# Kernel optimization log

Measured on AMD Instinct MI355X. Metric: run time of the kernel, lower is better.

The kernel has to match this reference:

```python
import jax, jax.numpy as jnp
import numpy as np

FREQUENCY_COUNT = 16

def setup_inputs() -> dict:
    key = jax.random.key(0)
    k1, k2 = jax.random.split(key)
    x = jax.random.normal(k1, (4096, 1024), dtype=jnp.float32)
    coef = jax.random.normal(k2, (1024, 1024, 2 * FREQUENCY_COUNT + 1), dtype=jnp.float32) * 0.1
    return {"x": x, "coef": coef}

def _fourier_features(x, K):
    ks = jnp.arange(1, K + 1, dtype=x.dtype)            # [K]
    ang = x[:, :, None] * ks[None, None, :]             # [B, I, K]
    ones = jnp.ones(x.shape + (1,), dtype=x.dtype)      # [B, I, 1]
    return jnp.concatenate([jnp.sin(ang), jnp.cos(ang), ones], axis=2)

def reference(x, coef):
    K = (coef.shape[-1] - 1) // 2
    values = _fourier_features(x, K)                     # [B, I, 2K+1]
    # sum over input dim i and frequency dim k, weighted per output j
    return jnp.einsum("oik,bik->bo", coef, values)      # [B, O]
```

## Files before the change

kernel.cpp:

```cpp
#include <hip/hip_runtime.h>


#define O_COLS 1024
#define I_DIM  1024
#define NF33   33
#define B_ROWS 4096

#define CW2_BYTES  ((size_t)32 * 2048 * 512 * 2)
#define XT_OFF     (CW2_BYTES)
#define XT_BYTES   ((size_t)I_DIM * B_ROWS * 4)
#define BK_OFF     (XT_OFF + XT_BYTES)
#define BK_BYTES   ((size_t)I_DIM * O_COLS * 4)
#define BIAS_OFF   (BK_OFF + BK_BYTES)
#define PART_OFF   (BIAS_OFF + (1 << 20))
#define PART_BYTES ((size_t)B_ROWS * O_COLS * 4)
#define NEED_T1    (PART_OFF + 3 * PART_BYTES)
#define NEED_T2    (BIAS_OFF + 4096)

#define ASTR 36

typedef _Float16 half8 __attribute__((ext_vector_type(8)));
typedef float f32x16 __attribute__((ext_vector_type(16)));
typedef float float4v __attribute__((ext_vector_type(4)));
union H8 { half8 v; _Float16 h[8]; };

#define BAR() asm volatile("s_waitcnt lgkmcnt(0)\n\ts_barrier" ::: "memory")

__device__ __forceinline__ int ksrc_of(int f) {
  return (f >= 32) ? 32 : ((f >> 1) + ((f & 1) ? 16 : 0));
}

__global__ __launch_bounds__(256)
void convert_coef2(const float* __restrict__ coef, _Float16* __restrict__ Cw2,
                   float* __restrict__ bk) {
  const int gtid = blockIdx.x * 256 + threadIdx.x;
  const int o = gtid & 1023;
  const int i = gtid >> 10;

  const float* src = coef + (size_t)o * (I_DIM * NF33) + (size_t)i * NF33;
  float r[NF33];
#pragma unroll
  for (int k = 0; k < NF33; ++k) r[k] = src[k];

  const int ob32 = o >> 5;
#pragma unroll
  for (int kcl = 0; kcl < 2; ++kcl) {
#pragma unroll
    for (int kh = 0; kh < 2; ++kh) {
      H8 h;
#pragma unroll
      for (int e = 0; e < 8; ++e)
        h.h[e] = (_Float16)r[ksrc_of(kcl * 16 + kh * 8 + e)];
      const size_t blob = (size_t)ob32 * 2048 + (size_t)i * 2 + kcl;
      *(half8*)(Cw2 + blob * 512 + (kh * 32 + (o & 31)) * 8) = h.v;
    }
  }
  bk[(size_t)i * 1024 + o] = r[32];
}

__global__ __launch_bounds__(256)
void transpose_x(const float* __restrict__ x, float* __restrict__ xT) {
  __shared__ float t[64][65];
  const int bi = blockIdx.x;
  const int bj = blockIdx.y;
  const int tx = threadIdx.x & 63, ty = threadIdx.x >> 6;
#pragma unroll
  for (int mq = 0; mq < 16; ++mq) {
    const int r = mq * 4 + ty;
    t[r][tx] = x[(size_t)(bj * 64 + r) * I_DIM + bi * 64 + tx];
  }
  __syncthreads();
#pragma unroll
  for (int mq = 0; mq < 16; ++mq) {
    const int r = mq * 4 + ty;
    xT[(size_t)(bi * 64 + r) * B_ROWS + bj * 64 + tx] = t[tx][r];
  }
}

__global__ __launch_bounds__(256)
void bias_from_bk(const float* __restrict__ bk, float* __restrict__ bias) {
  const int o = blockIdx.x * 256 + threadIdx.x;
  float s0 = 0.f, s1 = 0.f, s2 = 0.f, s3 = 0.f;
  for (int i = 0; i < 1024; i += 4) {
    s0 += bk[(size_t)i * 1024 + o];
    s1 += bk[(size_t)(i + 1) * 1024 + o];
    s2 += bk[(size_t)(i + 2) * 1024 + o];
    s3 += bk[(size_t)(i + 3) * 1024 + o];
  }
  bias[o] = (s0 + s1) + (s2 + s3);
}

__global__ __launch_bounds__(256)
void reduce_parts(float* __restrict__ out, const float* __restrict__ p0,
                  const float* __restrict__ p1, const float* __restrict__ p2) {
  const size_t i = ((size_t)blockIdx.x * 256 + threadIdx.x) * 4;
  float4v a = *(float4v*)(out + i);
  float4v b = *(const float4v*)(p0 + i);
  float4v c = *(const float4v*)(p1 + i);
  float4v d = *(const float4v*)(p2 + i);
  *(float4v*)(out + i) = a + b + c + d;
}

__device__ __forceinline__ void genH(float xv, _Float16* dst) {
  float S[17], C[17];
  __sincosf(xv, &S[1], &C[1]);
  S[2] = 2.f * S[1] * C[1];  C[2] = fmaf(-2.f * S[1], S[1], 1.f);
  S[3] = S[2] * C[1] + C[2] * S[1];  C[3] = C[2] * C[1] - S[2] * S[1];
  S[4] = 2.f * S[2] * C[2];  C[4] = fmaf(-2.f * S[2], S[2], 1.f);
  S[5] = S[4] * C[1] + C[4] * S[1];  C[5] = C[4] * C[1] - S[4] * S[1];
  S[6] = S[4] * C[2] + C[4] * S[2];  C[6] = C[4] * C[2] - S[4] * S[2];
  S[7] = S[4] * C[3] + C[4] * S[3];  C[7] = C[4] * C[3] - S[4] * S[3];
  S[8] = 2.f * S[4] * C[4];  C[8] = fmaf(-2.f * S[4], S[4], 1.f);
#pragma unroll
  for (int k = 1; k < 8; ++k) {
    S[8 + k] = S[8] * C[k] + C[8] * S[k];
    C[8 + k] = C[8] * C[k] - S[8] * S[k];
  }
  S[16] = 2.f * S[8] * C[8];  C[16] = fmaf(-2.f * S[8], S[8], 1.f);
#pragma unroll
  for (int c4 = 0; c4 < 4; ++c4) {
    H8 h;
#pragma unroll
    for (int q = 0; q < 4; ++q) {
      const int k = c4 * 4 + q + 1;
      h.h[2 * q] = (_Float16)S[k];  h.h[2 * q + 1] = (_Float16)C[k];
    }
    *(half8*)(dst + c4 * 8) = h.v;
  }
}

template <bool ATOMIC>
__global__ __launch_bounds__(384, 2)
void fourier_gemm10(const float* __restrict__ xT, const _Float16* __restrict__ Cw2,
                    const float* __restrict__ bias, float* __restrict__ out,
                    float* __restrict__ part) {
  __shared__ _Float16 As[2][4][128][ASTR];

  const int tid = threadIdx.x, lane = tid & 63, wave = tid >> 6;

  const int bid = blockIdx.x;
  const int g = bid & 15;
  const int m0 = (bid >> 4) * 128;
  const int n = g >> 2;
  const int kb = g & 3;
  const int o0 = n * 256;
  const int i0 = kb * 256;

  if (wave >= 4) {
    const int grow = tid - 256;
    const float* px = xT + (size_t)i0 * B_ROWS + (m0 + grow);

    {
      float x4[4];
#pragma unroll
      for (int c = 0; c < 4; ++c) x4[c] = px[(size_t)c * B_ROWS];
#pragma unroll
      for (int c = 0; c < 4; ++c) genH(x4[c], &As[0][c][grow][0]);
    }
    BAR();
#pragma unroll 1
    for (int p = 0; p < 64; ++p) {
      if (p < 63) {
        const int s1 = 4 * (p + 1);
        float x4[4];
#pragma unroll
        for (int c = 0; c < 4; ++c) x4[c] = px[(size_t)(s1 + c) * B_ROWS];
        _Float16* dstb = &As[(p & 1) ^ 1][0][grow][0];
#pragma unroll
        for (int c = 0; c < 4; ++c) genH(x4[c], dstb + c * (128 * ASTR));
      }
      BAR();
    }
    return;
  }

  const int wc = wave;
  const int r32 = lane & 31, kh = lane >> 5;

  const _Float16* pb0 = Cw2 + ((size_t)(n * 8 + wc * 2 + 0) * 2048 + (size_t)i0 * 2) * 512 + lane * 8;
  const _Float16* pb1 = Cw2 + ((size_t)(n * 8 + wc * 2 + 1) * 2048 + (size_t)i0 * 2) * 512 + lane * 8;

  f32x16 acc[4][2];
#pragma unroll
  for (int fr = 0; fr < 4; ++fr)
#pragma unroll
    for (int fc = 0; fc < 2; ++fc)
#pragma unroll
      for (int q = 0; q < 16; ++q) acc[fr][fc][q] = 0.f;
  if (kb == 0) {
#pragma unroll
    for (int fc = 0; fc < 2; ++fc) {
      const float bv = bias[o0 + wc * 64 + fc * 32 + r32];
#pragma unroll
      for (int fr = 0; fr < 4; ++fr)
#pragma unroll
        for (int q = 0; q < 16; ++q) acc[fr][fc][q] = bv;
    }
  }

  half8 B0[4], B1[4];
  auto loadB = [&](half8 (&Bt)[4], int s) {
    const size_t base = (size_t)(s * 2) * 512;
    Bt[0] = *(const half8*)(pb0 + base);
    Bt[1] = *(const half8*)(pb0 + base + 512);
    Bt[2] = *(const half8*)(pb1 + base);
    Bt[3] = *(const half8*)(pb1 + base + 512);
  };
  auto mfma_sub = [&](int buf, int col, const half8 (&Bt)[4]) {
    half8 a_[4][2];
#pragma unroll
    for (int fr = 0; fr < 4; ++fr)
#pragma unroll
      for (int kcl = 0; kcl < 2; ++kcl)
        a_[fr][kcl] = *(const half8*)&As[buf][col][fr * 32 + r32][(kcl * 2 + kh) * 8];
#pragma unroll
    for (int kcl = 0; kcl < 2; ++kcl)
#pragma unroll
      for (int fr = 0; fr < 4; ++fr)
#pragma unroll
        for (int fc = 0; fc < 2; ++fc)
          acc[fr][fc] = __builtin_amdgcn_mfma_f32_32x32x16_f16(
              a_[fr][kcl], Bt[fc * 2 + kcl], acc[fr][fc], 0, 0, 0);
  };

  loadB(B0, 0);
  BAR();

#pragma unroll 1
  for (int p = 0; p < 64; ++p) {
    const int buf = p & 1;
    const int s = 4 * p;
    loadB(B1, s + 1);
    mfma_sub(buf, 0, B0);
    loadB(B0, s + 2);
    mfma_sub(buf, 1, B1);
    loadB(B1, s + 3);
    mfma_sub(buf, 2, B0);
    if (p < 63) loadB(B0, s + 4);
    mfma_sub(buf, 3, B1);
    BAR();
  }

  float* dst;
  if (ATOMIC) dst = out;
  else dst = (kb == 0) ? out : part + (size_t)(kb - 1) * (B_ROWS * O_COLS);
#pragma unroll
  for (int fr = 0; fr < 4; ++fr)
#pragma unroll
    for (int fc = 0; fc < 2; ++fc)
#pragma unroll
      for (int q = 0; q < 16; ++q) {
        const int row = m0 + fr * 32 + (q & 3) + 8 * (q >> 2) + 4 * kh;
        const int col = o0 + wc * 64 + fc * 32 + r32;
        if (ATOMIC) atomicAdd(&dst[(size_t)row * O_COLS + col], acc[fr][fc][q]);
        else dst[(size_t)row * O_COLS + col] = acc[fr][fc][q];
      }
}

__global__ __launch_bounds__(512, 4)
void fourier_gemm_direct(const float* __restrict__ x, const float* __restrict__ coef,
                         float* __restrict__ out) {
  __shared__ _Float16 Asd[128 * 64];
  __shared__ _Float16 Bsd[128 * 64];

  const int tid = threadIdx.x;
  const int lane = tid & 63;
  const int wave = tid >> 6;
  const int wr = wave >> 1;
  const int wcd = wave & 1;

  const int bid = blockIdx.x;
  const int o0 = (bid & 7) * 128;
  const int kb = (bid >> 3) & 1;
  const int m0 = (bid >> 4) * 128;

  const int rowA = tid >> 3;
  const int cch = tid & 7;
  const int cswz = cch ^ (rowA & 7);
  const int n1 = tid >> 3;
  const int c1q = tid & 7;
  const int r16 = lane & 15;
  const int kq = lane >> 4;

  float4v acc[2][4];
#pragma unroll
  for (int fr = 0; fr < 2; ++fr)
#pragma unroll
    for (int fc = 0; fc < 4; ++fc) acc[fr][fc] = (float4v){0.f, 0.f, 0.f, 0.f};

  float s1a[8], c1a[8], sa[8], ca[8];
  float s1b[8], c1b[8], sb[8], cb[8];

  const float* xa_base = x + (size_t)(m0 + rowA) * I_DIM + (size_t)kb * 512 + cch * 8;
  const float* xb_base = xa_base + (size_t)64 * I_DIM;

#pragma unroll 1
  for (int ib2 = 0; ib2 < 8; ++ib2) {
    {
      const float* xa = xa_base + ib2 * 64;
      const float* xb = xb_base + ib2 * 64;
      float xva[8], xvb[8];
      *(float4*)&xva[0] = *(const float4*)(xa);
      *(float4*)&xva[4] = *(const float4*)(xa + 4);
      *(float4*)&xvb[0] = *(const float4*)(xb);
      *(float4*)&xvb[4] = *(const float4*)(xb + 4);
#pragma unroll
      for (int e = 0; e < 8; ++e) {
        __sincosf(xva[e], &s1a[e], &c1a[e]); sa[e] = s1a[e]; ca[e] = c1a[e];
        __sincosf(xvb[e], &s1b[e], &c1b[e]); sb[e] = s1b[e]; cb[e] = c1b[e];
      }
    }
#pragma unroll 1
    for (int f = 0; f < NF33; ++f) {
      H8 ha, hb;
      if (f == 32) {
#pragma unroll
        for (int e = 0; e < 8; ++e) { ha.h[e] = (_Float16)1.0f; hb.h[e] = (_Float16)1.0f; }
      } else if ((f & 1) == 0) {
#pragma unroll
        for (int e = 0; e < 8; ++e) { ha.h[e] = (_Float16)sa[e]; hb.h[e] = (_Float16)sb[e]; }
      } else {
#pragma unroll
        for (int e = 0; e < 8; ++e) { ha.h[e] = (_Float16)ca[e]; hb.h[e] = (_Float16)cb[e]; }
      }
      __syncthreads();
      {
        const int ks = ksrc_of(f);
        const int ibg = kb * 8 + ib2;
        H8 b1, b2;
#pragma unroll
        for (int e = 0; e < 8; ++e) {
          const size_t ii = (size_t)(ibg * 64 + c1q * 8 + e) * NF33 + ks;
          b1.h[e] = (_Float16)coef[(size_t)(o0 + n1) * (I_DIM * NF33) + ii];
          b2.h[e] = (_Float16)coef[(size_t)(o0 + n1 + 64) * (I_DIM * NF33) + ii];
        }
        const int cs = (c1q ^ (n1 & 7)) << 3;
        *(half8*)&Bsd[n1 * 64 + cs] = b1.v;
        *(half8*)&Bsd[(n1 + 64) * 64 + cs] = b2.v;
      }
      *(half8*)&Asd[rowA * 64 + cswz * 8] = ha.v;
      *(half8*)&Asd[(rowA + 64) * 64 + cswz * 8] = hb.v;
      if ((f & 1) && (f + 2 < NF33)) {
#pragma unroll
        for (int e = 0; e < 8; ++e) {
          float ns = sa[e] * c1a[e] + ca[e] * s1a[e];
          ca[e] = ca[e] * c1a[e] - sa[e] * s1a[e]; sa[e] = ns;
          float nsb = sb[e] * c1b[e] + cb[e] * s1b[e];
          cb[e] = cb[e] * c1b[e] - sb[e] * s1b[e]; sb[e] = nsb;
        }
      }
      __syncthreads();
#pragma unroll
      for (int ksu = 0; ksu < 2; ++ksu) {
        const int ch = ((ksu << 2) + kq) ^ (r16 & 7);
        half8 af[2], bf[4];
#pragma unroll
        for (int fr = 0; fr < 2; ++fr)
          af[fr] = *(const half8*)&Asd[(wr * 32 + fr * 16 + r16) * 64 + ch * 8];
#pragma unroll
        for (int fc = 0; fc < 4; ++fc)
          bf[fc] = *(const half8*)&Bsd[(wcd * 64 + fc * 16 + r16) * 64 + ch * 8];
#pragma unroll
        for (int fr = 0; fr < 2; ++fr)
#pragma unroll
          for (int fc = 0; fc < 4; ++fc)
            acc[fr][fc] = __builtin_amdgcn_mfma_f32_16x16x32_f16(
                af[fr], bf[fc], acc[fr][fc], 0, 0, 0);
      }
    }
  }
#pragma unroll
  for (int fr = 0; fr < 2; ++fr)
#pragma unroll
    for (int fc = 0; fc < 4; ++fc)
#pragma unroll
      for (int r = 0; r < 4; ++r) {
        const int row = m0 + wr * 32 + fr * 16 + kq * 4 + r;
        const int col = o0 + wcd * 64 + fc * 16 + r16;
        atomicAdd(&out[(size_t)row * O_COLS + col], acc[fr][fc][r]);
      }
}

extern "C" void kernel_launch(void* const* d_in, const int* in_sizes, int n_in,
                              void* d_out, int out_size, void* d_ws, size_t ws_size,
                              hipStream_t stream) {
  const float* x = (const float*)d_in[0];
  const float* coef = (const float*)d_in[1];
  float* out = (float*)d_out;

  if (ws_size >= NEED_T1 || ws_size >= NEED_T2) {
    _Float16* Cw2 = (_Float16*)d_ws;
    float* xT   = (float*)((char*)d_ws + XT_OFF);
    float* bk   = (float*)((char*)d_ws + BK_OFF);
    float* bias = (float*)((char*)d_ws + BIAS_OFF);
    convert_coef2<<<dim3(4096), dim3(256), 0, stream>>>(coef, Cw2, bk);
    transpose_x<<<dim3(16, 64), dim3(256), 0, stream>>>(x, xT);
    bias_from_bk<<<dim3(4), dim3(256), 0, stream>>>(bk, bias);
    if (ws_size >= NEED_T1) {
      float* part = (float*)((char*)d_ws + PART_OFF);
      fourier_gemm10<false><<<dim3(512), dim3(384), 0, stream>>>(xT, Cw2, bias, out, part);
      reduce_parts<<<dim3(4096), dim3(256), 0, stream>>>(
          out, part, part + (size_t)B_ROWS * O_COLS, part + (size_t)2 * B_ROWS * O_COLS);
    } else {
      hipMemsetAsync(out, 0, (size_t)B_ROWS * O_COLS * sizeof(float), stream);
      fourier_gemm10<true><<<dim3(512), dim3(384), 0, stream>>>(xT, Cw2, bias, out, nullptr);
    }
  } else {
    hipMemsetAsync(out, 0, (size_t)B_ROWS * O_COLS * sizeof(float), stream);
    fourier_gemm_direct<<<dim3(512), dim3(512), 0, stream>>>(x, coef, out);
  }
}
```

Before: 463.6 us.

## Merge feature-generation waves into MFMA waves and widen output tile

Removes the dedicated producer waves that computed Fourier features into shared memory. All eight waves now do MFMA work over a 512-column output tile, and each wave pair generates one feature column between its MFMA sub-steps, with x values prefetched one iteration ahead. The aim is to stop leaving two waves idle for matrix math and to reuse each A tile across twice as many output columns. The cost is higher register pressure at 512 threads per block and half as many blocks (256), which may leave CUs underfilled.

Result: faster. 422.3 us (-8.9%).

```diff
diff --git a/kernel.cpp b/kernel.cpp
--- a/kernel.cpp
+++ b/kernel.cpp
@@ -130,8 +130,8 @@
 }
 
 template <bool ATOMIC>
-__global__ __launch_bounds__(384, 2)
-void fourier_gemm10(const float* __restrict__ xT, const _Float16* __restrict__ Cw2,
+__global__ __launch_bounds__(512, 2)
+void fourier_gemm11(const float* __restrict__ xT, const _Float16* __restrict__ Cw2,
                     const float* __restrict__ bias, float* __restrict__ out,
                     float* __restrict__ part) {
   __shared__ _Float16 As[2][4][128][ASTR];
@@ -139,46 +139,22 @@
   const int tid = threadIdx.x, lane = tid & 63, wave = tid >> 6;
 
   const int bid = blockIdx.x;
-  const int g = bid & 15;
-  const int m0 = (bid >> 4) * 128;
-  const int n = g >> 2;
-  const int kb = g & 3;
-  const int o0 = n * 256;
+  const int g = bid & 7;
+  const int m0 = (bid >> 3) * 128;
+  const int n = g & 1;
+  const int kb = g >> 1;
+  const int o0 = n * 512;
   const int i0 = kb * 256;
 
-  if (wave >= 4) {
-    const int grow = tid - 256;
-    const float* px = xT + (size_t)i0 * B_ROWS + (m0 + grow);
-
-    {
-      float x4[4];
-#pragma unroll
-      for (int c = 0; c < 4; ++c) x4[c] = px[(size_t)c * B_ROWS];
-#pragma unroll
-      for (int c = 0; c < 4; ++c) genH(x4[c], &As[0][c][grow][0]);
-    }
-    BAR();
-#pragma unroll 1
-    for (int p = 0; p < 64; ++p) {
-      if (p < 63) {
-        const int s1 = 4 * (p + 1);
-        float x4[4];
-#pragma unroll
-        for (int c = 0; c < 4; ++c) x4[c] = px[(size_t)(s1 + c) * B_ROWS];
-        _Float16* dstb = &As[(p & 1) ^ 1][0][grow][0];
-#pragma unroll
-        for (int c = 0; c < 4; ++c) genH(x4[c], dstb + c * (128 * ASTR));
-      }
-      BAR();
-    }
-    return;
-  }
-
-  const int wc = wave;
   const int r32 = lane & 31, kh = lane >> 5;
-
-  const _Float16* pb0 = Cw2 + ((size_t)(n * 8 + wc * 2 + 0) * 2048 + (size_t)i0 * 2) * 512 + lane * 8;
-  const _Float16* pb1 = Cw2 + ((size_t)(n * 8 + wc * 2 + 1) * 2048 + (size_t)i0 * 2) * 512 + lane * 8;
+  const int gslot = wave >> 1;
+
+  const int grow = tid & 127;
+  const int gcol = tid >> 7;
+  const float* px = xT + (size_t)(i0 + gcol) * B_ROWS + (m0 + grow);
+
+  const _Float16* pb0 = Cw2 + ((size_t)(n * 16 + wave * 2 + 0) * 2048 + (size_t)i0 * 2) * 512 + lane * 8;
+  const _Float16* pb1 = Cw2 + ((size_t)(n * 16 + wave * 2 + 1) * 2048 + (size_t)i0 * 2) * 512 + lane * 8;
 
   f32x16 acc[4][2];
 #pragma unroll
@@ -190,7 +166,7 @@
   if (kb == 0) {
 #pragma unroll
     for (int fc = 0; fc < 2; ++fc) {
-      const float bv = bias[o0 + wc * 64 + fc * 32 + r32];
+      const float bv = bias[o0 + wave * 64 + fc * 32 + r32];
 #pragma unroll
       for (int fr = 0; fr < 4; ++fr)
 #pragma unroll
@@ -206,6 +182,7 @@
     Bt[2] = *(const half8*)(pb1 + base);
     Bt[3] = *(const half8*)(pb1 + base + 512);
   };
+
   auto mfma_sub = [&](int buf, int col, const half8 (&Bt)[4]) {
     half8 a_[4][2];
 #pragma unroll
@@ -223,6 +200,8 @@
               a_[fr][kcl], Bt[fc * 2 + kcl], acc[fr][fc], 0, 0, 0);
   };
 
+  genH(px[0], &As[0][gcol][grow][0]);
+  float xa = px[(size_t)4 * B_ROWS];
   loadB(B0, 0);
   BAR();
 
@@ -230,15 +209,23 @@
   for (int p = 0; p < 64; ++p) {
     const int buf = p & 1;
     const int s = 4 * p;
+    const float xan = px[(size_t)(s + 8) * B_ROWS];
+    _Float16* gdst = &As[buf ^ 1][gcol][grow][0];
+
     loadB(B1, s + 1);
     mfma_sub(buf, 0, B0);
+    if (gslot == 0) genH(xa, gdst);
     loadB(B0, s + 2);
     mfma_sub(buf, 1, B1);
+    if (gslot == 1) genH(xa, gdst);
     loadB(B1, s + 3);
     mfma_sub(buf, 2, B0);
+    if (gslot == 2) genH(xa, gdst);
     if (p < 63) loadB(B0, s + 4);
     mfma_sub(buf, 3, B1);
+    if (gslot == 3) genH(xa, gdst);
     BAR();
+    xa = xan;
   }
 
   float* dst;
@@ -251,7 +238,7 @@
 #pragma unroll
       for (int q = 0; q < 16; ++q) {
         const int row = m0 + fr * 32 + (q & 3) + 8 * (q >> 2) + 4 * kh;
-        const int col = o0 + wc * 64 + fc * 32 + r32;
+        const int col = o0 + wave * 64 + fc * 32 + r32;
         if (ATOMIC) atomicAdd(&dst[(size_t)row * O_COLS + col], acc[fr][fc][q]);
         else dst[(size_t)row * O_COLS + col] = acc[fr][fc][q];
       }
@@ -398,12 +385,12 @@
     bias_from_bk<<<dim3(4), dim3(256), 0, stream>>>(bk, bias);
     if (ws_size >= NEED_T1) {
       float* part = (float*)((char*)d_ws + PART_OFF);
-      fourier_gemm10<false><<<dim3(512), dim3(384), 0, stream>>>(xT, Cw2, bias, out, part);
+      fourier_gemm11<false><<<dim3(256), dim3(512), 0, stream>>>(xT, Cw2, bias, out, part);
       reduce_parts<<<dim3(4096), dim3(256), 0, stream>>>(
           out, part, part + (size_t)B_ROWS * O_COLS, part + (size_t)2 * B_ROWS * O_COLS);
     } else {
       hipMemsetAsync(out, 0, (size_t)B_ROWS * O_COLS * sizeof(float), stream);
-      fourier_gemm10<true><<<dim3(512), dim3(384), 0, stream>>>(xT, Cw2, bias, out, nullptr);
+      fourier_gemm11<true><<<dim3(256), dim3(512), 0, stream>>>(xT, Cw2, bias, out, nullptr);
     }
   } else {
     hipMemsetAsync(out, 0, (size_t)B_ROWS * O_COLS * sizeof(float), stream);
```
